# Kernel optimization log

Measured on AMD Instinct MI355X. Metric: run time of the kernel, lower is better.

Reference implementation:

```python
import jax, jax.numpy as jnp
import numpy as np

B, N, C = 4, 3136, 64
IMG_H = IMG_W = 56
HEADS = 1
TOPK = 8
HID = 4 * C  # mlp_ratio=4.0


def _ln(x, g, b, eps=1e-5):
    m = x.mean(-1, keepdims=True)
    v = ((x - m) ** 2).mean(-1, keepdims=True)
    return (x - m) * jax.lax.rsqrt(v + eps) * g + b


def _conv(x, w, b, pad, groups):
    y = jax.lax.conv_general_dilated(
        x, w, (1, 1), [(pad, pad), (pad, pad)],
        dimension_numbers=('NCHW', 'OIHW', 'NCHW'), feature_group_count=groups)
    return y + b[None, :, None, None]


def setup_inputs() -> dict:
    key = jax.random.key(0)
    ks = jax.random.split(key, 10)
    def rn(k, shp, scale=0.02):
        return jax.random.normal(k, shp, jnp.float32) * scale
    return {
        'x': jax.random.normal(ks[0], (B, N, C), jnp.float32),
        'norm1_g': jnp.ones((C,), jnp.float32), 'norm1_b': jnp.zeros((C,), jnp.float32),
        'wq': rn(ks[1], (C, C)), 'bq': jnp.zeros((C,), jnp.float32),
        'wkv': rn(ks[2], (C, 2 * C)), 'bkv': jnp.zeros((2 * C,), jnp.float32),
        'wproj': rn(ks[3], (C, C)), 'bproj': jnp.zeros((C,), jnp.float32),
        'local_w': rn(ks[4], (C, C // HEADS, 3, 3), 0.05), 'local_b': jnp.zeros((C,), jnp.float32),
        'norm2_g': jnp.ones((C,), jnp.float32), 'norm2_b': jnp.zeros((C,), jnp.float32),
        'w3': rn(ks[5], (HID, 1, 3, 3), 0.05), 'b3': jnp.zeros((HID,), jnp.float32),
        'w5': rn(ks[6], (HID, 1, 5, 5), 0.05), 'b5': jnp.zeros((HID,), jnp.float32),
        'w1': rn(ks[7], (C, 2 * HID, 1, 1), 0.05), 'b1': jnp.zeros((C,), jnp.float32),
        'H': IMG_H, 'W': IMG_W,
    }


def reference(x, norm1_g, norm1_b, wq, bq, wkv, bkv, wproj, bproj,
              local_w, local_b, norm2_g, norm2_b, w3, b3, w5, b5, w1, b1, H, W):
    Bb, Nn, Cc = x.shape
    d = Cc // HEADS
    scale = d ** -0.5
    # --- DynamicSparseAttention (global branch) ---
    xn = _ln(x, norm1_g, norm1_b)
    q = (xn @ wq + bq).reshape(Bb, Nn, HEADS, d).transpose(0, 2, 1, 3)       # bhnd
    kv = (xn @ wkv + bkv).reshape(Bb, Nn, 2, HEADS, d)
    k = kv[:, :, 0].transpose(0, 2, 1, 3)
    v = kv[:, :, 1].transpose(0, 2, 1, 3)
    attn = jnp.einsum('bhnd,bhmd->bhnm', q, k) * scale                        # [B,h,N,N]
    kth = jax.lax.top_k(attn, TOPK)[0][..., -1:]                              # k-th largest per row
    mask = (attn >= kth).astype(attn.dtype)                                   # top-k scatter mask
    p = jax.nn.softmax(attn * mask, axis=-1)                                  # zeros kept (as in torch ref)
    g = jnp.einsum('bhnm,bhmd->bhnd', p, v).transpose(0, 2, 1, 3).reshape(Bb, Nn, Cc)
    g = g @ wproj + bproj
    # --- local conv attention branch ---
    x_img = x.transpose(0, 2, 1).reshape(Bb, Cc, H, W)
    loc = _conv(x_img, local_w, local_b, 1, HEADS).reshape(Bb, Cc, Nn).transpose(0, 2, 1)
    # --- residual 1 (note: norm1 params reused, as in source) ---
    x = x + _ln(g + loc, norm1_g, norm1_b)
    # --- MSFN ---
    xn2 = _ln(x, norm2_g, norm2_b).transpose(0, 2, 1).reshape(Bb, Cc, H, W)
    x3 = _conv(xn2, w3, b3, 1, Cc)   # depthwise 3x3, channel mult 4
    x5 = _conv(xn2, w5, b5, 2, Cc)   # depthwise 5x5, channel mult 4
    m = _conv(jnp.concatenate([x3, x5], axis=1), w1, b1, 0, 1)
    return x + m.reshape(Bb, Cc, Nn).transpose(0, 2, 1)
```

## Files before the change

### kernel.cpp

```cpp
#include <hip/hip_runtime.h>
#include <math.h>

#define Bv 4
#define Nv 3136
#define Cv 64
#define Hh 56
#define Ww 56
#define HIDv 256
#define TOPKv 8
#define TSP 520
#define LCP 584
#define XNP 72
#define KSPL 16
#define KPS 196

constexpr float SCALE = 0.125f;
constexpr float EPS = 1e-5f;
constexpr float SBIAS = 128.0f;

typedef short bf16x8 __attribute__((ext_vector_type(8)));
typedef float f32x4 __attribute__((ext_vector_type(4)));

#define CSWAP(a, b) { unsigned int _hi = max(a, b); unsigned int _lo = min(a, b); a = _hi; b = _lo; }
#define BITONIC8(T) \
  CSWAP(T[0], T[4]); CSWAP(T[1], T[5]); CSWAP(T[2], T[6]); CSWAP(T[3], T[7]); \
  CSWAP(T[0], T[2]); CSWAP(T[1], T[3]); CSWAP(T[4], T[6]); CSWAP(T[5], T[7]); \
  CSWAP(T[0], T[1]); CSWAP(T[2], T[3]); CSWAP(T[4], T[5]); CSWAP(T[6], T[7]);

__device__ __forceinline__ unsigned short f2bf(float f) {
  unsigned int u = __float_as_uint(f);
  u = (u + 0x7FFFu + ((u >> 16) & 1u)) >> 16;
  return (unsigned short)u;
}
__device__ __forceinline__ float bf2f(unsigned short u) {
  return __uint_as_float(((unsigned int)u) << 16);
}
__device__ __forceinline__ unsigned int pack2(float a, float b) {
  return (unsigned int)f2bf(a) | ((unsigned int)f2bf(b) << 16);
}

__device__ __forceinline__ unsigned int packB(float sb, int j) {
  return (__float_as_uint(sb) & 0xFFFFF000u) | (unsigned int)j;
}

__global__ void k_transpose(const float* __restrict__ w1, const float* __restrict__ lw,
                            const float* __restrict__ w3, const float* __restrict__ w5,
                            const float* __restrict__ wq, const float* __restrict__ wkv,
                            const float* __restrict__ bq, const float* __restrict__ bkv,
                            const float* __restrict__ wproj,
                            unsigned short* __restrict__ w1bf, unsigned short* __restrict__ lwb,
                            float* __restrict__ w3t, float* __restrict__ w5t,
                            unsigned short* __restrict__ wqkvt, float* __restrict__ qkvb,
                            unsigned short* __restrict__ wprojt, float* __restrict__ sumv) {
  int p = blockIdx.x * 256 + threadIdx.x;
  if (p < 256) sumv[p] = 0.0f;
  if (p < 64 * 512) w1bf[p] = f2bf(w1[p]);
  if (p < 64 * 576) {
    int co = p / 576, k = p % 576;
    int tap = k >> 6, ci = k & 63;
    lwb[p] = f2bf(lw[co * 576 + ci * 9 + tap]);
  }
  if (p < 36 * 64) {
    int cin = p & 63, tm = p >> 6;
    int tap = tm >> 2, m = tm & 3;
    w3t[p] = w3[(cin * 4 + m) * 9 + tap];
  }
  if (p < 100 * 64) {
    int cin = p & 63, tm = p >> 6;
    int tap = tm >> 2, m = tm & 3;
    w5t[p] = w5[(cin * 4 + m) * 25 + tap];
  }
  if (p < 192 * 64) {
    int o = p >> 6, i = p & 63;
    float v = (o < 64) ? wq[i * 64 + o] : wkv[i * 128 + (o - 64)];
    wqkvt[p] = f2bf(v);
  }
  if (p < 192) qkvb[p] = (p < 64) ? bq[p] : bkv[p - 64];
  if (p < 64 * 64) {
    int o = p >> 6, i = p & 63;
    wprojt[p] = f2bf(wproj[i * 64 + o]);
  }
}

__global__ __launch_bounds__(256) void k_ln_qkv(
    const float* __restrict__ x, const float* __restrict__ g1, const float* __restrict__ b1,
    const unsigned short* __restrict__ wqkvt, const float* __restrict__ qkvb,
    unsigned short* __restrict__ q16, unsigned short* __restrict__ k16,
    float* __restrict__ vo, float* __restrict__ sumv) {
  __shared__ __align__(16) unsigned short xnS[16 * XNP];
  int bid = blockIdx.x;
  int b = bid / 196, tile = bid % 196;
  size_t tok0 = (size_t)b * Nv + tile * 16;
  int t = threadIdx.x;
  int w = t >> 6, l = t & 63;
  int tokL = t >> 4;
  int ch0 = (t & 15) * 4;
  size_t tok = tok0 + tokL;
  float v[4];
  *(float4*)v = *(const float4*)&x[tok * 64 + ch0];
  float s = v[0] + v[1] + v[2] + v[3];
  float s2 = v[0] * v[0] + v[1] * v[1] + v[2] * v[2] + v[3] * v[3];
#pragma unroll
  for (int off = 1; off <= 8; off <<= 1) {
    s += __shfl_xor(s, off, 64);
    s2 += __shfl_xor(s2, off, 64);
  }
  float m = s * (1.f / 64.f);
  float rs = rsqrtf(s2 * (1.f / 64.f) - m * m + EPS);
  {
    unsigned int pk[2];
    float a0_ = (v[0] - m) * rs * g1[ch0] + b1[ch0];
    float a1_ = (v[1] - m) * rs * g1[ch0 + 1] + b1[ch0 + 1];
    float a2_ = (v[2] - m) * rs * g1[ch0 + 2] + b1[ch0 + 2];
    float a3_ = (v[3] - m) * rs * g1[ch0 + 3] + b1[ch0 + 3];
    pk[0] = pack2(a0_, a1_);
    pk[1] = pack2(a2_, a3_);
    *(uint2*)&xnS[tokL * XNP + ch0] = *(uint2*)pk;
  }
  __syncthreads();
  int n = l & 15, q = l >> 4;
  const bf16x8 a0 = *(const bf16x8*)&xnS[n * XNP + q * 8];
  const bf16x8 a1 = *(const bf16x8*)&xnS[n * XNP + 32 + q * 8];
  {
    const unsigned short* wr = &wqkvt[(size_t)(w * 16 + n) * 64];
    bf16x8 b0 = *(const bf16x8*)&wr[q * 8];
    bf16x8 b1_ = *(const bf16x8*)&wr[32 + q * 8];
    f32x4 acc = {0.f, 0.f, 0.f, 0.f};
    acc = __builtin_amdgcn_mfma_f32_16x16x32_bf16(a0, b0, acc, 0, 0, 0);
    acc = __builtin_amdgcn_mfma_f32_16x16x32_bf16(a1, b1_, acc, 0, 0, 0);
    float bias = qkvb[w * 16 + n];
#pragma unroll
    for (int r = 0; r < 4; ++r)
      q16[(tok0 + q * 4 + r) * 64 + w * 16 + n] = f2bf(acc[r] + bias);
  }
  {
    const unsigned short* wr = &wqkvt[(size_t)((w + 4) * 16 + n) * 64];
    bf16x8 b0 = *(const bf16x8*)&wr[q * 8];
    bf16x8 b1_ = *(const bf16x8*)&wr[32 + q * 8];
    f32x4 acc = {0.f, 0.f, 0.f, 0.f};
    acc = __builtin_amdgcn_mfma_f32_16x16x32_bf16(a0, b0, acc, 0, 0, 0);
    acc = __builtin_amdgcn_mfma_f32_16x16x32_bf16(a1, b1_, acc, 0, 0, 0);
    float bias = qkvb[64 + w * 16 + n];
#pragma unroll
    for (int r = 0; r < 4; ++r)
      k16[(tok0 + q * 4 + r) * 64 + w * 16 + n] = f2bf(acc[r] + bias);
  }
  {
    const unsigned short* wr = &wqkvt[(size_t)((w + 8) * 16 + n) * 64];
    bf16x8 b0 = *(const bf16x8*)&wr[q * 8];
    bf16x8 b1_ = *(const bf16x8*)&wr[32 + q * 8];
    f32x4 acc = {0.f, 0.f, 0.f, 0.f};
    acc = __builtin_amdgcn_mfma_f32_16x16x32_bf16(a0, b0, acc, 0, 0, 0);
    acc = __builtin_amdgcn_mfma_f32_16x16x32_bf16(a1, b1_, acc, 0, 0, 0);
    float bias = qkvb[128 + w * 16 + n];
    float vp = acc[0] + acc[1] + acc[2] + acc[3] + 4.0f * bias;
#pragma unroll
    for (int r = 0; r < 4; ++r)
      vo[(tok0 + q * 4 + r) * 64 + w * 16 + n] = acc[r] + bias;
    vp += __shfl_xor(vp, 16, 64);
    vp += __shfl_xor(vp, 32, 64);
    if (q == 0) atomicAdd(&sumv[b * 64 + w * 16 + n], vp);
  }
}

#define PAIRMERGE(T, accA, accB, jb) { \
    unsigned int _p0 = packB(accA[0], (jb) + 0); \
    unsigned int _p1 = packB(accA[1], (jb) + 1); \
    unsigned int _p2 = packB(accA[2], (jb) + 2); \
    unsigned int _p3 = packB(accA[3], (jb) + 3); \
    unsigned int _q0 = packB(accB[0], (jb) + 16); \
    unsigned int _q1 = packB(accB[1], (jb) + 17); \
    unsigned int _q2 = packB(accB[2], (jb) + 18); \
    unsigned int _q3 = packB(accB[3], (jb) + 19); \
    CSWAP(_p0, _p1); CSWAP(_p2, _p3); CSWAP(_p0, _p2); CSWAP(_p1, _p3); CSWAP(_p1, _p2); \
    CSWAP(_q0, _q1); CSWAP(_q2, _q3); CSWAP(_q0, _q2); CSWAP(_q1, _q3); CSWAP(_q1, _q2); \
    unsigned int _u8[8] = {_p0, _p1, _p2, _p3, _q3, _q2, _q1, _q0}; \
    BITONIC8(_u8); \
    T[0] = max(T[0], _u8[7]); \
    T[1] = max(T[1], _u8[6]); \
    T[2] = max(T[2], _u8[5]); \
    T[3] = max(T[3], _u8[4]); \
    T[4] = max(T[4], _u8[3]); \
    T[5] = max(T[5], _u8[2]); \
    T[6] = max(T[6], _u8[1]); \
    T[7] = max(T[7], _u8[0]); \
    BITONIC8(T); }

__global__ __launch_bounds__(256, 4) void k_attn_topk(
    const unsigned short* __restrict__ q16, const unsigned short* __restrict__ k16,
    unsigned int* __restrict__ top8out) {
  __shared__ __align__(16) unsigned short kS[13312];
  int bid = blockIdx.x;
  int t = threadIdx.x;
  int w = t >> 6;
  int lane = t & 63;
  int tgq = bid % 25;
  int bs = bid / 25;
  int b = bs >> 4, split = bs & 15;
  int tg2 = tgq * 4 + w;
  size_t bN = (size_t)b * Nv;
  int kbase = split * KPS;

  {
    const char* src = (const char*)(k16 + bN * 64) + kbase * 128 + t * 16;
    char* dst = (char*)kS + (t >> 3) * 128 + (((t & 7) ^ ((t >> 3) & 7)) << 4);
#pragma unroll
    for (int r = 0; r < 6; ++r)
      *(uint4*)(dst + r * 4096) = *(const uint4*)(src + r * 4096);
    if (t < 128)
      *(uint4*)(dst + 6 * 4096) = *(const uint4*)(src + 6 * 4096);
  }
  __syncthreads();
  if (tg2 >= 98) return;

  int qbase = b * Nv + tg2 * 32;
  int qcol = lane & 15, quad = lane >> 4;
  int quad4 = quad * 4;
  int m = lane & 15;

  bf16x8 qf0a[2], qf1a[2];
#pragma unroll
  for (int tt = 0; tt < 2; ++tt) {
    qf0a[tt] = *(const bf16x8*)&q16[((size_t)(qbase + tt * 16 + qcol)) * 64 + quad * 8];
    qf1a[tt] = *(const bf16x8*)&q16[((size_t)(qbase + tt * 16 + qcol)) * 64 + 32 + quad * 8];
  }

  unsigned int t8[2][8];
#pragma unroll
  for (int tt = 0; tt < 2; ++tt)
#pragma unroll
    for (int u = 0; u < 8; ++u) t8[tt][u] = 0u;

  int jbA = kbase + quad4;
  int swz = m & 7;
  const char* pa = (const char*)kS + m * 128 + ((quad ^ swz) << 4);
  const char* pb = (const char*)kS + m * 128 + (((quad + 4) ^ swz) << 4);

#pragma unroll 1
  for (int it = 0; it < 6; ++it) {
    bf16x8 ca0 = *(const bf16x8*)(pa + it * 4096);
    bf16x8 ca1 = *(const bf16x8*)(pb + it * 4096);
    bf16x8 cb0 = *(const bf16x8*)(pa + it * 4096 + 2048);
    bf16x8 cb1 = *(const bf16x8*)(pb + it * 4096 + 2048);

#pragma unroll
    for (int tt = 0; tt < 2; ++tt) {
      f32x4 accA = {SBIAS, SBIAS, SBIAS, SBIAS};
      accA = __builtin_amdgcn_mfma_f32_16x16x32_bf16(ca0, qf0a[tt], accA, 0, 0, 0);
      accA = __builtin_amdgcn_mfma_f32_16x16x32_bf16(ca1, qf1a[tt], accA, 0, 0, 0);
      f32x4 accB = {SBIAS, SBIAS, SBIAS, SBIAS};
      accB = __builtin_amdgcn_mfma_f32_16x16x32_bf16(cb0, qf0a[tt], accB, 0, 0, 0);
      accB = __builtin_amdgcn_mfma_f32_16x16x32_bf16(cb1, qf1a[tt], accB, 0, 0, 0);
      PAIRMERGE(t8[tt], accA, accB, jbA);
    }
    jbA += 32;
  }

  {
    bf16x8 ka0 = *(const bf16x8*)(pa + 12 * 2048);
    bf16x8 ka1 = *(const bf16x8*)(pb + 12 * 2048);
    int klim = kbase + KPS;
#pragma unroll
    for (int tt = 0; tt < 2; ++tt) {
      f32x4 accA = {SBIAS, SBIAS, SBIAS, SBIAS};
      accA = __builtin_amdgcn_mfma_f32_16x16x32_bf16(ka0, qf0a[tt], accA, 0, 0, 0);
      accA = __builtin_amdgcn_mfma_f32_16x16x32_bf16(ka1, qf1a[tt], accA, 0, 0, 0);
      unsigned int p0 = (jbA + 0 < klim) ? packB(accA[0], jbA + 0) : 0u;
      unsigned int p1 = (jbA + 1 < klim) ? packB(accA[1], jbA + 1) : 0u;
      unsigned int p2 = (jbA + 2 < klim) ? packB(accA[2], jbA + 2) : 0u;
      unsigned int p3 = (jbA + 3 < klim) ? packB(accA[3], jbA + 3) : 0u;
      CSWAP(p0, p1); CSWAP(p2, p3); CSWAP(p0, p2); CSWAP(p1, p3); CSWAP(p1, p2);
      t8[tt][4] = max(t8[tt][4], p3);
      t8[tt][5] = max(t8[tt][5], p2);
      t8[tt][6] = max(t8[tt][6], p1);
      t8[tt][7] = max(t8[tt][7], p0);
      BITONIC8(t8[tt]);
    }
  }

#pragma unroll
  for (int tt = 0; tt < 2; ++tt) {
#pragma unroll
    for (int step = 16; step <= 32; step <<= 1) {
      unsigned int o[8];
#pragma unroll
      for (int i = 0; i < 8; ++i) o[i] = (unsigned int)__shfl_xor((int)t8[tt][i], step, 64);
      unsigned int nw[8];
#pragma unroll
      for (int i = 0; i < 8; ++i) nw[i] = max(t8[tt][i], o[7 - i]);
#pragma unroll
      for (int i = 0; i < 8; ++i) t8[tt][i] = nw[i];
      BITONIC8(t8[tt]);
    }
    if (quad == 0) {
      size_t obase = ((size_t)(bN + tg2 * 32 + tt * 16 + qcol)) * 128 + split * 8;
      *(uint4*)&top8out[obase] = make_uint4(t8[tt][0], t8[tt][1], t8[tt][2], t8[tt][3]);
      *(uint4*)&top8out[obase + 4] = make_uint4(t8[tt][4], t8[tt][5], t8[tt][6], t8[tt][7]);
    }
  }
}

__global__ __launch_bounds__(256) void k_attn_proj(
    const unsigned int* __restrict__ top8, const float* __restrict__ vg,
    const float* __restrict__ sumv, const float* __restrict__ x,
    const unsigned short* __restrict__ lwb, const float* __restrict__ lb,
    const unsigned short* __restrict__ wprojt, const float* __restrict__ bproj,
    const float* __restrict__ g1, const float* __restrict__ b1,
    const float* __restrict__ g2, const float* __restrict__ b2,
    float* __restrict__ x2, unsigned short* __restrict__ xn2b) {
  __shared__ float kwS[16][8];
  __shared__ int kidxS[16][8];
  __shared__ float invZS[16];
  __shared__ __align__(16) unsigned short imS[16 * LCP];
  __shared__ __align__(16) unsigned short gS[16 * XNP];
  __shared__ float yS[16 * 66];
  int bid = blockIdx.x;
  int b = bid / 196, rem = bid % 196;
  int th = rem / 7, tw = rem % 7;
  int h0 = th * 2, w0 = tw * 8;
  size_t bN = (size_t)b * Nv;
  int t = threadIdx.x;

  if (t < 64) {
    int tk = t >> 2, la = t & 3;
    int gtok = (h0 + (tk >> 3)) * Ww + w0 + (tk & 7);
    size_t base = (bN + gtok) * 128 + la * 32;
    unsigned int A[8];
#pragma unroll
    for (int i = 0; i < 8; ++i) A[i] = top8[base + i];
#pragma unroll
    for (int h = 1; h < 4; ++h) {
      unsigned int Bb[8];
#pragma unroll
      for (int i = 0; i < 8; ++i) Bb[i] = top8[base + h * 8 + i];
#pragma unroll
      for (int i = 0; i < 8; ++i) A[i] = max(A[i], Bb[7 - i]);
      BITONIC8(A);
    }
#pragma unroll
    for (int step = 1; step <= 2; step <<= 1) {
      unsigned int o[8];
#pragma unroll
      for (int i = 0; i < 8; ++i) o[i] = (unsigned int)__shfl_xor((int)A[i], step, 64);
#pragma unroll
      for (int i = 0; i < 8; ++i) A[i] = max(A[i], o[7 - i]);
      BITONIC8(A);
    }
    if (la == 0) {
      float Z = (float)(Nv - TOPKv);
#pragma unroll
      for (int u = 0; u < 8; ++u) {
        float sb = __uint_as_float(A[u] & 0xFFFFF000u);
        float s = (sb - SBIAS) * SCALE;
        float e = __expf(s);
        kwS[tk][u] = e - 1.0f;
        kidxS[tk][u] = (int)(A[u] & 0xFFFu);
        Z += e;
      }
      invZS[tk] = 1.0f / Z;
    }
  } else {
    for (int p = t - 64; p < 1152; p += 192) {
      int sub = p & 7, s = p >> 3;
      int tok = s / 9, tap = s % 9;
      int tr = tok >> 3, tc = tok & 7;
      int dh = tap / 3, dw = tap % 3;
      int gh = h0 + tr - 1 + dh, gw = w0 + tc - 1 + dw;
      uint4 uu = {0u, 0u, 0u, 0u};
      if (gh >= 0 && gh < Hh && gw >= 0 && gw < Ww) {
        const float* xp = &x[(bN + gh * Ww + gw) * 64 + sub * 8];
        float4 va = *(const float4*)xp;
        float4 vb = *(const float4*)(xp + 4);
        uu.x = pack2(va.x, va.y);
        uu.y = pack2(va.z, va.w);
        uu.z = pack2(vb.x, vb.y);
        uu.w = pack2(vb.z, vb.w);
      }
      *(uint4*)&imS[tok * LCP + tap * 64 + sub * 8] = uu;
    }
  }
  __syncthreads();

  int w = t >> 6, l = t & 63;
  int n = l & 15, q = l >> 4;

  int c = t & 63, rg = t >> 6;
  float vgv[4][8];
#pragma unroll
  for (int rr = 0; rr < 4; ++rr) {
    int tokL = rg * 4 + rr;
#pragma unroll
    for (int u = 0; u < 8; ++u)
      vgv[rr][u] = vg[(bN + kidxS[tokL][u]) * 64 + c];
  }

  f32x4 lacc = {0.f, 0.f, 0.f, 0.f};
  {
    const unsigned short* lwrow = &lwb[(size_t)(w * 16 + n) * 576];
#pragma unroll 6
    for (int kk = 0; kk < 18; ++kk) {
      bf16x8 af = *(const bf16x8*)&imS[n * LCP + kk * 32 + q * 8];
      bf16x8 bfr = *(const bf16x8*)&lwrow[kk * 32 + q * 8];
      lacc = __builtin_amdgcn_mfma_f32_16x16x32_bf16(af, bfr, lacc, 0, 0, 0);
    }
  }
  float lbias = lb[w * 16 + n];

  {
    float sv = sumv[b * 64 + c];
#pragma unroll
    for (int rr = 0; rr < 4; ++rr) {
      int tokL = rg * 4 + rr;
      float acc = sv;
#pragma unroll
      for (int u = 0; u < 8; ++u)
        acc += kwS[tokL][u] * vgv[rr][u];
      gS[tokL * XNP + c] = f2bf(acc * invZS[tokL]);
    }
  }
  __syncthreads();

  {
    const bf16x8 a0 = *(const bf16x8*)&gS[n * XNP + q * 8];
    const bf16x8 a1 = *(const bf16x8*)&gS[n * XNP + 32 + q * 8];
    const unsigned short* wr = &wprojt[(size_t)(w * 16 + n) * 64];
    bf16x8 b0 = *(const bf16x8*)&wr[q * 8];
    bf16x8 b1_ = *(const bf16x8*)&wr[32 + q * 8];
    f32x4 acc = {0.f, 0.f, 0.f, 0.f};
    acc = __builtin_amdgcn_mfma_f32_16x16x32_bf16(a0, b0, acc, 0, 0, 0);
    acc = __builtin_amdgcn_mfma_f32_16x16x32_bf16(a1, b1_, acc, 0, 0, 0);
    float bias = bproj[w * 16 + n];
#pragma unroll
    for (int r = 0; r < 4; ++r)
      yS[(q * 4 + r) * 66 + w * 16 + n] = acc[r] + bias + lacc[r] + lbias;
  }
  __syncthreads();

  int tokL = t >> 4;
  int ch0 = (t & 15) * 4;
  size_t tok = bN + (size_t)(h0 + (tokL >> 3)) * Ww + w0 + (tokL & 7);
  float y[4];
#pragma unroll
  for (int i = 0; i < 4; ++i) y[i] = yS[tokL * 66 + ch0 + i];
  float s = y[0] + y[1] + y[2] + y[3];
  float s2 = y[0] * y[0] + y[1] * y[1] + y[2] * y[2] + y[3] * y[3];
#pragma unroll
  for (int off = 1; off <= 8; off <<= 1) {
    s += __shfl_xor(s, off, 64);
    s2 += __shfl_xor(s2, off, 64);
  }
  float m1 = s * (1.f / 64.f);
  float rs1 = rsqrtf(s2 * (1.f / 64.f) - m1 * m1 + EPS);
  float xv[4];
  *(float4*)xv = *(const float4*)&x[tok * 64 + ch0];
  float x2v[4];
  float t_s = 0.f, t_s2 = 0.f;
#pragma unroll
  for (int i = 0; i < 4; ++i) {
    float t1 = (y[i] - m1) * rs1 * g1[ch0 + i] + b1[ch0 + i];
    x2v[i] = xv[i] + t1;
    t_s += x2v[i];
    t_s2 += x2v[i] * x2v[i];
  }
#pragma unroll
  for (int off = 1; off <= 8; off <<= 1) {
    t_s += __shfl_xor(t_s, off, 64);
    t_s2 += __shfl_xor(t_s2, off, 64);
  }
  float m2 = t_s * (1.f / 64.f);
  float rs2 = rsqrtf(t_s2 * (1.f / 64.f) - m2 * m2 + EPS);
  *(float4*)&x2[tok * 64 + ch0] = *(float4*)x2v;
  unsigned int pk[2];
  {
    float a0_ = (x2v[0] - m2) * rs2 * g2[ch0] + b2[ch0];
    float a1_ = (x2v[1] - m2) * rs2 * g2[ch0 + 1] + b2[ch0 + 1];
    float a2_ = (x2v[2] - m2) * rs2 * g2[ch0 + 2] + b2[ch0 + 2];
    float a3_ = (x2v[3] - m2) * rs2 * g2[ch0 + 3] + b2[ch0 + 3];
    pk[0] = pack2(a0_, a1_);
    pk[1] = pack2(a2_, a3_);
  }
  *(uint2*)&xn2b[tok * 64 + ch0] = *(uint2*)pk;
}

__global__ __launch_bounds__(256) void k_msfn(
    const unsigned short* __restrict__ xn2b, const float* __restrict__ x2,
    const float* __restrict__ w3t, const float* __restrict__ b3,
    const float* __restrict__ w5t, const float* __restrict__ b5,
    const unsigned short* __restrict__ w1bf, const float* __restrict__ b1,
    float* __restrict__ out) {
  __shared__ __align__(16) unsigned short xtS[6 * 12 * 64];
  __shared__ __align__(16) unsigned short tsS[16 * TSP];

  int bid = blockIdx.x;
  int b = bid / 196;
  int rem = bid % 196;
  int th = rem / 7, tw = rem % 7;
  int h0 = th * 2, w0 = tw * 8;
  size_t bN = (size_t)b * Nv;
  int t = threadIdx.x;

  unsigned int* xtU = (unsigned int*)xtS;
  for (int p = t; p < 6 * 12 * 32; p += 256) {
    int cp = p & 31, rc = p >> 5;
    int r = rc / 12, cc = rc % 12;
    int gh = h0 - 2 + r, gw = w0 - 2 + cc;
    unsigned int v = 0;
    if (gh >= 0 && gh < Hh && gw >= 0 && gw < Ww)
      v = *(const unsigned int*)&xn2b[(bN + gh * Ww + gw) * 64 + cp * 2];
    xtU[rc * 32 + cp] = v;
  }
  __syncthreads();

  int cin = t & 63, tg = t >> 6;
  int tr = tg >> 1, tc0 = (tg & 1) * 4;
  float win[5][8];
#pragma unroll
  for (int r = 0; r < 5; ++r)
#pragma unroll
    for (int c = 0; c < 8; ++c)
      win[r][c] = bf2f(xtS[((tr + r) * 12 + tc0 + c) * 64 + cin]);

  unsigned int* tsU = (unsigned int*)tsS;
#pragma unroll 1
  for (int m2 = 0; m2 < 4; m2 += 2) {
    float a3[2][9], a5[2][25], bb3[2], bb5[2];
#pragma unroll
    for (int mm = 0; mm < 2; ++mm) {
      int m = m2 + mm;
#pragma unroll
      for (int tap = 0; tap < 9; ++tap) a3[mm][tap] = w3t[(tap * 4 + m) * 64 + cin];
#pragma unroll
      for (int tap = 0; tap < 25; ++tap) a5[mm][tap] = w5t[(tap * 4 + m) * 64 + cin];
      bb3[mm] = b3[cin * 4 + m];
      bb5[mm] = b5[cin * 4 + m];
    }
#pragma unroll
    for (int tk = 0; tk < 4; ++tk) {
      int tok = tg * 4 + tk;
      unsigned int p3 = 0, p5 = 0;
#pragma unroll
      for (int mm = 0; mm < 2; ++mm) {
        float acc3 = bb3[mm];
#pragma unroll
        for (int kh = 0; kh < 3; ++kh)
#pragma unroll
          for (int kw2 = 0; kw2 < 3; ++kw2)
            acc3 += win[1 + kh][tk + 1 + kw2] * a3[mm][kh * 3 + kw2];
        float acc5 = bb5[mm];
#pragma unroll
        for (int kh = 0; kh < 5; ++kh)
#pragma unroll
          for (int kw2 = 0; kw2 < 5; ++kw2)
            acc5 += win[kh][tk + kw2] * a5[mm][kh * 5 + kw2];
        p3 |= (unsigned int)f2bf(acc3) << (16 * mm);
        p5 |= (unsigned int)f2bf(acc5) << (16 * mm);
      }
      tsU[(tok * TSP + cin * 4 + m2) >> 1] = p3;
      tsU[(tok * TSP + 256 + cin * 4 + m2) >> 1] = p5;
    }
  }
  __syncthreads();

  int wv = tg, lane = t & 63;
  int n16 = lane & 15, quad = lane >> 4;
  const unsigned short* wrow = &w1bf[(size_t)(wv * 16 + n16) * 512];
  f32x4 acc = {0.f, 0.f, 0.f, 0.f};
#pragma unroll 4
  for (int kk = 0; kk < 16; ++kk) {
    bf16x8 af = *(const bf16x8*)&tsS[n16 * TSP + kk * 32 + quad * 8];
    bf16x8 bfr = *(const bf16x8*)&wrow[kk * 32 + quad * 8];
    acc = __builtin_amdgcn_mfma_f32_16x16x32_bf16(af, bfr, acc, 0, 0, 0);
  }
  float bias = b1[wv * 16 + n16];
#pragma unroll
  for (int r = 0; r < 4; ++r) {
    int tok = quad * 4 + r;
    int trr = tok >> 3, tcc = tok & 7;
    size_t idx = (bN + (size_t)(h0 + trr) * Ww + w0 + tcc) * 64 + wv * 16 + n16;
    out[idx] = x2[idx] + acc[r] + bias;
  }
}

extern "C" void kernel_launch(void* const* d_in, const int* in_sizes, int n_in,
                              void* d_out, int out_size, void* d_ws, size_t ws_size,
                              hipStream_t stream) {
  const float* x = (const float*)d_in[0];
  const float* n1g = (const float*)d_in[1];
  const float* n1b = (const float*)d_in[2];
  const float* wq = (const float*)d_in[3];
  const float* bq = (const float*)d_in[4];
  const float* wkv = (const float*)d_in[5];
  const float* bkv = (const float*)d_in[6];
  const float* wproj = (const float*)d_in[7];
  const float* bproj = (const float*)d_in[8];
  const float* lw = (const float*)d_in[9];
  const float* lb = (const float*)d_in[10];
  const float* n2g = (const float*)d_in[11];
  const float* n2b = (const float*)d_in[12];
  const float* w3 = (const float*)d_in[13];
  const float* b3 = (const float*)d_in[14];
  const float* w5 = (const float*)d_in[15];
  const float* b5 = (const float*)d_in[16];
  const float* w1 = (const float*)d_in[17];
  const float* b1 = (const float*)d_in[18];
  float* out = (float*)d_out;

  float* ws = (float*)d_ws;
  const size_t TOK = (size_t)Bv * Nv * Cv;
  float* vb = ws;
  float* sumv = vb + TOK;
  float* x2 = sumv + 256;
  float* w3t = x2 + TOK;
  float* w5t = w3t + 2304;
  float* qkvb = w5t + 6400;
  unsigned short* q16 = (unsigned short*)(qkvb + 192);
  unsigned short* k16 = q16 + TOK;
  unsigned short* xn2b = k16 + TOK;
  unsigned short* w1bf = xn2b + TOK;
  unsigned short* lwb = w1bf + 64 * 512;
  unsigned short* wqkvt = lwb + 64 * 576;
  unsigned short* wprojt = wqkvt + 192 * 64;
  unsigned int* top8ws = (unsigned int*)(wprojt + 64 * 64 + 64);

  k_transpose<<<144, 256, 0, stream>>>(w1, lw, w3, w5, wq, wkv, bq, bkv, wproj,
                                       w1bf, lwb, w3t, w5t, wqkvt, qkvb, wprojt, sumv);
  k_ln_qkv<<<Bv * 196, 256, 0, stream>>>(x, n1g, n1b, wqkvt, qkvb, q16, k16, vb, sumv);
  k_attn_topk<<<Bv * 16 * 25, 256, 0, stream>>>(q16, k16, top8ws);
  k_attn_proj<<<Bv * 196, 256, 0, stream>>>(top8ws, vb, sumv, x, lwb, lb, wprojt, bproj,
                                            n1g, n1b, n2g, n2b, x2, xn2b);
  k_msfn<<<Bv * 196, 256, 0, stream>>>(xn2b, x2, w3t, b3, w5t, b5, w1bf, b1, out);
}
```

Measured before the change: 169.0 us.

## Use 512-thread blocks in top-k attention with one 16-query tile per wave

The attention top-k kernel now launches 512 threads per block, and each of its 8 waves handles a single 16-query tile instead of two. The shared K chunk is still loaded once per block, now spread over twice as many threads. This halves per-wave register state (one top-8 list and one Q fragment) so more waves can be resident, increasing latency hiding. In exchange, each K fragment read from LDS feeds only one MFMA pair instead of two, doubling LDS read traffic per query.

```diff
diff --git a/kernel.cpp b/kernel.cpp
--- a/kernel.cpp
+++ b/kernel.cpp
@@ -186,7 +186,7 @@
     T[7] = max(T[7], _u8[0]); \
     BITONIC8(T); }
 
-__global__ __launch_bounds__(256, 4) void k_attn_topk(
+__global__ __launch_bounds__(512, 6) void k_attn_topk(
     const unsigned short* __restrict__ q16, const unsigned short* __restrict__ k16,
     unsigned int* __restrict__ top8out) {
   __shared__ __align__(16) unsigned short kS[13312];
@@ -197,7 +197,7 @@
   int tgq = bid % 25;
   int bs = bid / 25;
   int b = bs >> 4, split = bs & 15;
-  int tg2 = tgq * 4 + w;
+  int tile = tgq * 8 + w;
   size_t bN = (size_t)b * Nv;
   int kbase = split * KPS;
 
@@ -205,31 +205,25 @@
     const char* src = (const char*)(k16 + bN * 64) + kbase * 128 + t * 16;
     char* dst = (char*)kS + (t >> 3) * 128 + (((t & 7) ^ ((t >> 3) & 7)) << 4);
 #pragma unroll
-    for (int r = 0; r < 6; ++r)
-      *(uint4*)(dst + r * 4096) = *(const uint4*)(src + r * 4096);
+    for (int r = 0; r < 3; ++r)
+      *(uint4*)(dst + r * 8192) = *(const uint4*)(src + r * 8192);
     if (t < 128)
-      *(uint4*)(dst + 6 * 4096) = *(const uint4*)(src + 6 * 4096);
+      *(uint4*)(dst + 3 * 8192) = *(const uint4*)(src + 3 * 8192);
   }
   __syncthreads();
-  if (tg2 >= 98) return;
-
-  int qbase = b * Nv + tg2 * 32;
+  if (tile >= 196) return;
+
+  int qbase = b * Nv + tile * 16;
   int qcol = lane & 15, quad = lane >> 4;
   int quad4 = quad * 4;
   int m = lane & 15;
 
-  bf16x8 qf0a[2], qf1a[2];
-#pragma unroll
-  for (int tt = 0; tt < 2; ++tt) {
-    qf0a[tt] = *(const bf16x8*)&q16[((size_t)(qbase + tt * 16 + qcol)) * 64 + quad * 8];
-    qf1a[tt] = *(const bf16x8*)&q16[((size_t)(qbase + tt * 16 + qcol)) * 64 + 32 + quad * 8];
-  }
-
-  unsigned int t8[2][8];
-#pragma unroll
-  for (int tt = 0; tt < 2; ++tt)
-#pragma unroll
-    for (int u = 0; u < 8; ++u) t8[tt][u] = 0u;
+  const bf16x8 qf0 = *(const bf16x8*)&q16[((size_t)(qbase + qcol)) * 64 + quad * 8];
+  const bf16x8 qf1 = *(const bf16x8*)&q16[((size_t)(qbase + qcol)) * 64 + 32 + quad * 8];
+
+  unsigned int t8[8];
+#pragma unroll
+  for (int u = 0; u < 8; ++u) t8[u] = 0u;
 
   int jbA = kbase + quad4;
   int swz = m & 7;
@@ -243,16 +237,13 @@
     bf16x8 cb0 = *(const bf16x8*)(pa + it * 4096 + 2048);
     bf16x8 cb1 = *(const bf16x8*)(pb + it * 4096 + 2048);
 
-#pragma unroll
-    for (int tt = 0; tt < 2; ++tt) {
-      f32x4 accA = {SBIAS, SBIAS, SBIAS, SBIAS};
-      accA = __builtin_amdgcn_mfma_f32_16x16x32_bf16(ca0, qf0a[tt], accA, 0, 0, 0);
-      accA = __builtin_amdgcn_mfma_f32_16x16x32_bf16(ca1, qf1a[tt], accA, 0, 0, 0);
-      f32x4 accB = {SBIAS, SBIAS, SBIAS, SBIAS};
-      accB = __builtin_amdgcn_mfma_f32_16x16x32_bf16(cb0, qf0a[tt], accB, 0, 0, 0);
-      accB = __builtin_amdgcn_mfma_f32_16x16x32_bf16(cb1, qf1a[tt], accB, 0, 0, 0);
-      PAIRMERGE(t8[tt], accA, accB, jbA);
-    }
+    f32x4 accA = {SBIAS, SBIAS, SBIAS, SBIAS};
+    accA = __builtin_amdgcn_mfma_f32_16x16x32_bf16(ca0, qf0, accA, 0, 0, 0);
+    accA = __builtin_amdgcn_mfma_f32_16x16x32_bf16(ca1, qf1, accA, 0, 0, 0);
+    f32x4 accB = {SBIAS, SBIAS, SBIAS, SBIAS};
+    accB = __builtin_amdgcn_mfma_f32_16x16x32_bf16(cb0, qf0, accB, 0, 0, 0);
+    accB = __builtin_amdgcn_mfma_f32_16x16x32_bf16(cb1, qf1, accB, 0, 0, 0);
+    PAIRMERGE(t8, accA, accB, jbA);
     jbA += 32;
   }
 
@@ -260,43 +251,37 @@
     bf16x8 ka0 = *(const bf16x8*)(pa + 12 * 2048);
     bf16x8 ka1 = *(const bf16x8*)(pb + 12 * 2048);
     int klim = kbase + KPS;
-#pragma unroll
-    for (int tt = 0; tt < 2; ++tt) {
-      f32x4 accA = {SBIAS, SBIAS, SBIAS, SBIAS};
-      accA = __builtin_amdgcn_mfma_f32_16x16x32_bf16(ka0, qf0a[tt], accA, 0, 0, 0);
-      accA = __builtin_amdgcn_mfma_f32_16x16x32_bf16(ka1, qf1a[tt], accA, 0, 0, 0);
-      unsigned int p0 = (jbA + 0 < klim) ? packB(accA[0], jbA + 0) : 0u;
-      unsigned int p1 = (jbA + 1 < klim) ? packB(accA[1], jbA + 1) : 0u;
-      unsigned int p2 = (jbA + 2 < klim) ? packB(accA[2], jbA + 2) : 0u;
-      unsigned int p3 = (jbA + 3 < klim) ? packB(accA[3], jbA + 3) : 0u;
-      CSWAP(p0, p1); CSWAP(p2, p3); CSWAP(p0, p2); CSWAP(p1, p3); CSWAP(p1, p2);
-      t8[tt][4] = max(t8[tt][4], p3);
-      t8[tt][5] = max(t8[tt][5], p2);
-      t8[tt][6] = max(t8[tt][6], p1);
-      t8[tt][7] = max(t8[tt][7], p0);
-      BITONIC8(t8[tt]);
-    }
-  }
-
-#pragma unroll
-  for (int tt = 0; tt < 2; ++tt) {
-#pragma unroll
-    for (int step = 16; step <= 32; step <<= 1) {
-      unsigned int o[8];
-#pragma unroll
-      for (int i = 0; i < 8; ++i) o[i] = (unsigned int)__shfl_xor((int)t8[tt][i], step, 64);
-      unsigned int nw[8];
-#pragma unroll
-      for (int i = 0; i < 8; ++i) nw[i] = max(t8[tt][i], o[7 - i]);
-#pragma unroll
-      for (int i = 0; i < 8; ++i) t8[tt][i] = nw[i];
-      BITONIC8(t8[tt]);
-    }
-    if (quad == 0) {
-      size_t obase = ((size_t)(bN + tg2 * 32 + tt * 16 + qcol)) * 128 + split * 8;
-      *(uint4*)&top8out[obase] = make_uint4(t8[tt][0], t8[tt][1], t8[tt][2], t8[tt][3]);
-      *(uint4*)&top8out[obase + 4] = make_uint4(t8[tt][4], t8[tt][5], t8[tt][6], t8[tt][7]);
-    }
+    f32x4 accA = {SBIAS, SBIAS, SBIAS, SBIAS};
+    accA = __builtin_amdgcn_mfma_f32_16x16x32_bf16(ka0, qf0, accA, 0, 0, 0);
+    accA = __builtin_amdgcn_mfma_f32_16x16x32_bf16(ka1, qf1, accA, 0, 0, 0);
+    unsigned int p0 = (jbA + 0 < klim) ? packB(accA[0], jbA + 0) : 0u;
+    unsigned int p1 = (jbA + 1 < klim) ? packB(accA[1], jbA + 1) : 0u;
+    unsigned int p2 = (jbA + 2 < klim) ? packB(accA[2], jbA + 2) : 0u;
+    unsigned int p3 = (jbA + 3 < klim) ? packB(accA[3], jbA + 3) : 0u;
+    CSWAP(p0, p1); CSWAP(p2, p3); CSWAP(p0, p2); CSWAP(p1, p3); CSWAP(p1, p2);
+    t8[4] = max(t8[4], p3);
+    t8[5] = max(t8[5], p2);
+    t8[6] = max(t8[6], p1);
+    t8[7] = max(t8[7], p0);
+    BITONIC8(t8);
+  }
+
+#pragma unroll
+  for (int step = 16; step <= 32; step <<= 1) {
+    unsigned int o[8];
+#pragma unroll
+    for (int i = 0; i < 8; ++i) o[i] = (unsigned int)__shfl_xor((int)t8[i], step, 64);
+    unsigned int nw[8];
+#pragma unroll
+    for (int i = 0; i < 8; ++i) nw[i] = max(t8[i], o[7 - i]);
+#pragma unroll
+    for (int i = 0; i < 8; ++i) t8[i] = nw[i];
+    BITONIC8(t8);
+  }
+  if (quad == 0) {
+    size_t obase = ((size_t)(bN + tile * 16 + qcol)) * 128 + split * 8;
+    *(uint4*)&top8out[obase] = make_uint4(t8[0], t8[1], t8[2], t8[3]);
+    *(uint4*)&top8out[obase + 4] = make_uint4(t8[4], t8[5], t8[6], t8[7]);
   }
 }
 
@@ -625,7 +610,7 @@
   k_transpose<<<144, 256, 0, stream>>>(w1, lw, w3, w5, wq, wkv, bq, bkv, wproj,
                                        w1bf, lwb, w3t, w5t, wqkvt, qkvb, wprojt, sumv);
   k_ln_qkv<<<Bv * 196, 256, 0, stream>>>(x, n1g, n1b, wqkvt, qkvb, q16, k16, vb, sumv);
-  k_attn_topk<<<Bv * 16 * 25, 256, 0, stream>>>(q16, k16, top8ws);
+  k_attn_topk<<<Bv * 16 * 25, 512, 0, stream>>>(q16, k16, top8ws);
   k_attn_proj<<<Bv * 196, 256, 0, stream>>>(top8ws, vb, sumv, x, lwb, lb, wprojt, bproj,
                                             n1g, n1b, n2g, n2b, x2, xn2b);
   k_msfn<<<Bv * 196, 256, 0, stream>>>(xn2b, x2, w3t, b3, w5t, b5, w1bf, b1, out);
```

New measurement: 170.1 us. About the same (+0.7%).
